# Kernel optimization log

Measured on AMD Instinct MI355X. Metric: run time of the kernel, lower is better.

The kernel has to match this reference:

```python
import jax, jax.numpy as jnp
import numpy as np

T = 5       # fixed temporal factor in the original forward
HEADS = 8
DIM = 512
DIM_HEAD = 64
INNER = HEADS * DIM_HEAD  # 512 (must equal DIM for the masked scatter)


def setup_inputs() -> dict:
    key = jax.random.key(0)
    ks = jax.random.split(key, 8)
    bt, n = 40, 3137  # b=8, t=5; n-1 = 56*56 visual tokens
    x = jax.random.normal(ks[0], (bt, n, DIM), dtype=jnp.float32)
    mask = jax.random.randint(ks[1], (bt, 56, 56), 0, 2).astype(jnp.float32)
    s = 1.0 / np.sqrt(DIM)
    w_vq = jax.random.normal(ks[2], (DIM, INNER), dtype=jnp.float32) * s
    w_vkv = jax.random.normal(ks[3], (DIM, 2 * INNER), dtype=jnp.float32) * s
    w_aqkv = jax.random.normal(ks[4], (DIM, 3 * INNER), dtype=jnp.float32) * s
    w_out = jax.random.normal(ks[5], (INNER, DIM), dtype=jnp.float32) * s
    b_out = jnp.zeros((DIM,), dtype=jnp.float32)
    return {"x": x, "mask": mask, "w_vq": w_vq, "w_vkv": w_vkv,
            "w_aqkv": w_aqkv, "w_out": w_out, "b_out": b_out}


def reference(x, mask, w_vq, w_vkv, w_aqkv, w_out, b_out):
    bt, n, dim = x.shape
    b = bt // T
    nv = n - 1
    dh = DIM_HEAD
    scale = dh ** -0.5

    A = x[:, 0]        # (bt, dim) -- single 'action' token per frame
    V = x[:, 1:]       # (bt, nv, dim)
    m = mask.reshape(bt, nv, 1)

    aq, ak, av = jnp.split(A @ w_aqkv, 3, axis=-1)      # each (bt, INNER)
    vk, vv = jnp.split(V @ w_vkv, 2, axis=-1)           # each (bt, nv, INNER)
    vq = V @ w_vq                                        # (bt, nv, INNER)

    # --- A -> V cross attention: per batch, T A-queries over T*nv V keys ---
    qa = aq.reshape(b, T, HEADS, dh)
    Kv = vk.reshape(b, T * nv, HEADS, dh)
    Vv = vv.reshape(b, T * nv, HEADS, dh)
    av_dots = jnp.einsum('bqhd,bkhd->bhqk', qa, Kv) * scale
    av_attn = jax.nn.softmax(av_dots, axis=-1)
    av_o = jnp.einsum('bhqk,bkhd->bqhd', av_attn, Vv)   # (b, T, H, dh)
    a_out = av_o.reshape(bt, 1, INNER)

    # --- V -> A cross attention with block mask: every V token attends only
    # to its own batch's T A-tokens (the -inf block fill in the original) ---
    Qv = vq.reshape(b, T, nv, HEADS, dh)
    Ka = ak.reshape(b, T, HEADS, dh)
    Va = av.reshape(b, T, HEADS, dh)
    va_dots = jnp.einsum('bfnhd,bkhd->bhfnk', Qv, Ka) * scale
    va_attn = jax.nn.softmax(va_dots, axis=-1)          # softmax over T keys
    va_o = jnp.einsum('bhfnk,bkhd->bfnhd', va_attn, Va)
    v_full = va_o.reshape(bt, nv, INNER)

    # original: scatter attn out into V.clone() then * mask, under no_grad()
    # => masked positions get attention output, others V*0 = 0; detached.
    v_out = jax.lax.stop_gradient(v_full * m)

    out = jnp.concatenate([a_out, v_out], axis=1)       # (bt, n, INNER)
    return out @ w_out + b_out
```

## Files before the change

kernel.cpp:

```cpp
#include <hip/hip_runtime.h>

typedef unsigned short u16;
typedef unsigned int u32;
typedef __attribute__((ext_vector_type(8))) u16 u16x8;
typedef __attribute__((ext_vector_type(8))) __bf16 bf16x8;
typedef __attribute__((ext_vector_type(4))) float f32x4;

__device__ __forceinline__ float b2f(u16 u){ return __uint_as_float(((u32)u)<<16); }
__device__ __forceinline__ u16 f2b(float f){
  u32 b = __float_as_uint(f);
  return (u16)((b + 0x7fffu + ((b>>16)&1u))>>16);
}
__device__ __forceinline__ void gload16(const void* g, void* l){
  __builtin_amdgcn_global_load_lds((__attribute__((address_space(1))) void*)g,
                                   (__attribute__((address_space(3))) void*)l, 16, 0, 0);
}
__device__ __forceinline__ float wred_max(float v){
#pragma unroll
  for (int o=32;o>0;o>>=1) v = fmaxf(v, __shfl_xor(v,o));
  return v;
}
__device__ __forceinline__ float wred_sum(float v){
#pragma unroll
  for (int o=32;o>0;o>>=1) v += __shfl_xor(v,o);
  return v;
}

__global__ void k_cast_x(const float* __restrict__ x, u16* __restrict__ xb, int n8){
  int stride = gridDim.x*blockDim.x;
  for (int i = blockIdx.x*blockDim.x + threadIdx.x; i < n8; i += stride){
    const float4* p = (const float4*)(x + (size_t)i*8);
    float4 a = p[0], b = p[1];
    u16x8 o;
    o[0]=f2b(a.x); o[1]=f2b(a.y); o[2]=f2b(a.z); o[3]=f2b(a.w);
    o[4]=f2b(b.x); o[5]=f2b(b.y); o[6]=f2b(b.z); o[7]=f2b(b.w);
    *(u16x8*)(xb + (size_t)i*8) = o;
  }
}

__global__ void k_prep_w(const float* __restrict__ wvq, const float* __restrict__ wvkv,
                         const float* __restrict__ wout, u16* __restrict__ W1T,
                         u16* __restrict__ WoutT){
  int id = blockIdx.x*blockDim.x + threadIdx.x;
  if (id < 786432){
    int n = id >> 9, k = id & 511;
    float v = (n < 512) ? wvq[k*512 + n] : wvkv[k*1024 + (n-512)];
    W1T[id] = f2b(v);
  } else {
    int j = id - 786432;
    int n = j >> 9, k = j & 511;
    WoutT[j] = f2b(wout[k*512 + n]);
  }
}

__global__ void k_agent_qkv(const float* __restrict__ x, const float* __restrict__ w,
                            float* __restrict__ aqkv){
  int id = blockIdx.x*blockDim.x + threadIdx.x;
  int bt = id / 1536, c = id % 1536;
  const float* xr = x + (size_t)bt*3137*512;
  float s = 0.f;
  for (int k=0;k<512;k++) s += xr[k]*w[k*1536+c];
  aqkv[id] = s;
}

template<int FOUT>
__global__ __launch_bounds__(512, 2) void k_gemm256(
    const u16* __restrict__ A, const u16* __restrict__ BT,
    int M, int N, int K, int NX,
    u16* __restrict__ Cb, float* __restrict__ Cf, const float* __restrict__ bias)
{
  __shared__ __align__(16) char Ls[4][32768];
  const int tid = threadIdx.x;
  const int wid = tid >> 6, lane = tid & 63;
  const int nwg = gridDim.x, orig = blockIdx.x;
  const int q8 = nwg >> 3, r8 = nwg & 7;
  const int xc = orig & 7, sl = orig >> 3;
  const int work = (xc < r8 ? xc*(q8+1) : r8*(q8+1) + (xc-r8)*q8) + sl;
  const int m0 = (work / NX) * 256, n0 = (work % NX) * 256;
  const size_t K2 = (size_t)K * 2;
  const char* Ab = (const char*)A;
  const char* Bb = (const char*)BT;
  size_t asrc[2], bsrc[2];
  const int ad0 = wid*1024, ad1 = 8192 + wid*1024;
#pragma unroll
  for (int i=0;i<2;i++){
    int row = (i*8 + wid)*16 + (lane & 15);
    int koff = (lane >> 4) << 4;
    int ra = m0 + row; if (ra >= M) ra = M - 1;
    asrc[i] = (size_t)ra * K2 + koff;
    bsrc[i] = (size_t)(n0 + row) * K2 + koff;
  }
#define STAGE(s4, ks) { \
    size_t ko = (size_t)(ks) * 64; \
    gload16(Ab + asrc[0] + ko, Ls[s4] + ad0); \
    gload16(Ab + asrc[1] + ko, Ls[s4] + ad1); \
    gload16(Bb + bsrc[0] + ko, Ls[s4] + 16384 + ad0); \
    gload16(Bb + bsrc[1] + ko, Ls[s4] + 16384 + ad1); }

  f32x4 acc[8][4] = {};
  const int awb = (wid >> 2) * 8192;
  const int bwb = 16384 + (wid & 3) * 4096;
  const int NS = K >> 5;
  STAGE(0,0) STAGE(1,1) STAGE(2,2)
  for (int s = 0; s < NS; ++s){
    if (s + 2 < NS)      { asm volatile("s_waitcnt vmcnt(8)" ::: "memory"); }
    else if (s + 1 < NS) { asm volatile("s_waitcnt vmcnt(4)" ::: "memory"); }
    else                 { asm volatile("s_waitcnt vmcnt(0)" ::: "memory"); }
    __builtin_amdgcn_s_barrier();
    __builtin_amdgcn_sched_barrier(0);
    if (s + 3 < NS) STAGE((s+3)&3, s+3)
    const char* base = Ls[s & 3];
    bf16x8 af[8], bfr[4];
#pragma unroll
    for (int i=0;i<4;i++) af[i] = *(const bf16x8*)(base + awb + i*1024 + lane*16);
#pragma unroll
    for (int i=0;i<4;i++) bfr[i] = *(const bf16x8*)(base + bwb + i*1024 + lane*16);
    asm volatile("s_waitcnt lgkmcnt(0)" ::: "memory");
    __builtin_amdgcn_sched_barrier(0);
    __builtin_amdgcn_s_setprio(1);
#pragma unroll
    for (int mr=0;mr<4;mr++)
#pragma unroll
      for (int nc=0;nc<4;nc++)
        acc[mr][nc] = __builtin_amdgcn_mfma_f32_16x16x32_bf16(af[mr], bfr[nc], acc[mr][nc], 0,0,0);
    __builtin_amdgcn_s_setprio(0);
#pragma unroll
    for (int i=4;i<8;i++) af[i] = *(const bf16x8*)(base + awb + i*1024 + lane*16);
    asm volatile("s_waitcnt lgkmcnt(0)" ::: "memory");
    __builtin_amdgcn_sched_barrier(0);
    __builtin_amdgcn_s_setprio(1);
#pragma unroll
    for (int mr=4;mr<8;mr++)
#pragma unroll
      for (int nc=0;nc<4;nc++)
        acc[mr][nc] = __builtin_amdgcn_mfma_f32_16x16x32_bf16(af[mr], bfr[nc], acc[mr][nc], 0,0,0);
    __builtin_amdgcn_s_setprio(0);
  }
#undef STAGE
  const int wm = (wid >> 2) * 128, wn = (wid & 3) * 64;
  if (m0 + 256 <= M){
#pragma unroll
    for (int mr=0;mr<8;mr++){
#pragma unroll
      for (int nc=0;nc<4;nc++){
#pragma unroll
        for (int rg=0;rg<4;rg++){
          int row = m0 + wm + mr*16 + ((lane>>4)<<2) + rg;
          int col = n0 + wn + nc*16 + (lane&15);
          float v = acc[mr][nc][rg];
          if (FOUT) Cf[(size_t)row*N + col] = v + bias[col];
          else      Cb[(size_t)row*N + col] = f2b(v);
        }
      }
    }
  } else {
#pragma unroll
    for (int mr=0;mr<8;mr++){
#pragma unroll
      for (int nc=0;nc<4;nc++){
#pragma unroll
        for (int rg=0;rg<4;rg++){
          int row = m0 + wm + mr*16 + ((lane>>4)<<2) + rg;
          int col = n0 + wn + nc*16 + (lane&15);
          if (row < M){
            float v = acc[mr][nc][rg];
            if (FOUT) Cf[(size_t)row*N + col] = v + bias[col];
            else      Cb[(size_t)row*N + col] = f2b(v);
          }
        }
      }
    }
  }
}

__global__ __launch_bounds__(320) void k_attn_agent(
    const u16* __restrict__ out1, const float* __restrict__ aqkv,
    float* __restrict__ pm, float* __restrict__ pl, float* __restrict__ pacc)
{
  __shared__ __align__(16) char Ksm[16384];
  __shared__ __align__(16) char Vsm[16384];
  const int bid = blockIdx.x;
  const int sp = bid & 15, bh = bid >> 4, b = bh >> 3, h = bh & 7;
  const int tid = threadIdx.x, wid = tid >> 6, lane = tid & 63;
  const int q = wid;
  float qreg[64];
  {
    const float* ap = aqkv + ((size_t)(b*5+q)*1536 + h*64);
#pragma unroll
    for (int d=0; d<64; d++) qreg[d] = ap[d];
  }
  float m = -1e30f, l = 0.f;
  float acc[8] = {0,0,0,0,0,0,0,0};
  const int g0 = sp * 980;
  for (int c = 0; c < 8; c++){
    for (int idx = tid; idx < 2048; idx += 320){
      int arr = idx >> 10, rem = idx & 1023;
      int r = rem >> 3, seg = rem & 7;
      int loc = c*128 + r; if (loc > 979) loc = 979;
      int gk = g0 + loc;
      int tk = gk / 3136, nv = gk - tk*3136;
      size_t grow = (size_t)((b*5+tk)*3137 + 1 + nv)*1536 + (arr ? 1024 : 512) + h*64 + seg*8;
      u16x8 v = *(const u16x8*)(out1 + grow);
      char* dst = arr ? Vsm : Ksm;
      *(u16x8*)(dst + r*128 + ((seg*16) ^ ((r&7)<<4))) = v;
    }
    __syncthreads();
    float s0 = 0.f, s1 = 0.f;
#pragma unroll
    for (int seg=0; seg<8; seg++){
      const int r0 = lane, r1 = 64 + lane;
      u16x8 k0 = *(const u16x8*)(Ksm + r0*128 + ((seg*16) ^ ((r0&7)<<4)));
      u16x8 k1 = *(const u16x8*)(Ksm + r1*128 + ((seg*16) ^ ((r1&7)<<4)));
#pragma unroll
      for (int j=0;j<8;j++){
        s0 += qreg[seg*8+j]*b2f(k0[j]);
        s1 += qreg[seg*8+j]*b2f(k1[j]);
      }
    }
    s0 *= 0.125f; s1 *= 0.125f;
    const int locbase = c*128;
    if (locbase + lane >= 980)      s0 = -1e30f;
    if (locbase + 64 + lane >= 980) s1 = -1e30f;
    float cmax = wred_max(fmaxf(s0, s1));
    float mn = fmaxf(m, cmax);
    float resc = __expf(m - mn);
    float p0 = (s0 > -1e29f) ? __expf(s0 - mn) : 0.f;
    float p1 = (s1 > -1e29f) ? __expf(s1 - mn) : 0.f;
    l = l*resc + wred_sum(p0 + p1);
#pragma unroll
    for (int j=0;j<8;j++) acc[j] *= resc;
    const int g = lane >> 3, cc = lane & 7;
#pragma unroll
    for (int i=0;i<16;i++){
      int k = i*8 + g;
      u16x8 vv = *(const u16x8*)(Vsm + k*128 + ((cc*16) ^ ((k&7)<<4)));
      float p = (i < 8) ? __shfl(p0, k) : __shfl(p1, k-64);
#pragma unroll
      for (int j=0;j<8;j++) acc[j] += p*b2f(vv[j]);
    }
    m = mn;
    __syncthreads();
  }
#pragma unroll
  for (int j=0;j<8;j++){
    float v = acc[j];
    v += __shfl_xor(v, 8); v += __shfl_xor(v, 16); v += __shfl_xor(v, 32);
    acc[j] = v;
  }
  const int base = (bh*16 + sp)*5 + q;
  if (lane == 0){ pm[base] = m; pl[base] = l; }
  if (lane < 8){
    float* pa = pacc + (size_t)base*64 + lane*8;
#pragma unroll
    for (int j=0;j<8;j++) pa[j] = acc[j];
  }
}

__global__ void k_agent_combine(const float* __restrict__ pm, const float* __restrict__ pl,
                                const float* __restrict__ pacc, u16* __restrict__ IN)
{
  const int id = blockIdx.x;
  const int q = id % 5, t2 = id / 5;
  const int h = t2 & 7, b = t2 >> 3;
  const int d = threadIdx.x;
  const int bh = b*8 + h;
  float ms = -1e30f;
#pragma unroll
  for (int s2=0;s2<16;s2++) ms = fmaxf(ms, pm[(bh*16+s2)*5+q]);
  float L = 0.f, o = 0.f;
#pragma unroll
  for (int s2=0;s2<16;s2++){
    int base = (bh*16+s2)*5+q;
    float w = __expf(pm[base]-ms);
    L += w*pl[base];
    o += w*pacc[(size_t)base*64 + d];
  }
  IN[(size_t)(b*5+q)*3137*512 + h*64 + d] = f2b(o / L);
}

__global__ __launch_bounds__(256) void k_attn_frame(
    const u16* __restrict__ out1, const float* __restrict__ aqkv,
    const float* __restrict__ mask, u16* __restrict__ IN)
{
  __shared__ float Ka[5][8][68];
  __shared__ float Va[5][8][68];
  const int b = blockIdx.y;
  const int tid = threadIdx.x;
  for (int i = tid; i < 2560; i += 256){
    int t = i >> 9, rem = i & 511, hh = rem >> 6, d = rem & 63;
    const float* src = aqkv + (size_t)(b*5+t)*1536;
    Ka[t][hh][d] = src[512 + hh*64 + d];
    Va[t][hh][d] = src[1024 + hh*64 + d];
  }
  __syncthreads();
  const int task = blockIdx.x*256 + tid;
  const int h = task & 7, rl = task >> 3;
  const int f = rl / 3136, nv = rl - f*3136;
  const int bt = b*5 + f;
  const size_t r1 = (size_t)bt*3137 + 1 + nv;
  const u16* qp = out1 + r1*1536 + h*64;
  float qf[64];
#pragma unroll
  for (int sg=0; sg<8; sg++){
    u16x8 v = *(const u16x8*)(qp + sg*8);
#pragma unroll
    for (int j=0;j<8;j++) qf[sg*8+j] = b2f(v[j]);
  }
  float sd[5];
#pragma unroll
  for (int t=0;t<5;t++){
    float s = 0.f;
#pragma unroll
    for (int d=0;d<64;d++) s += qf[d]*Ka[t][h][d];
    sd[t] = s*0.125f;
  }
  float mx = sd[0];
#pragma unroll
  for (int t=1;t<5;t++) mx = fmaxf(mx, sd[t]);
  float p[5], ps = 0.f;
#pragma unroll
  for (int t=0;t<5;t++){ p[t] = __expf(sd[t]-mx); ps += p[t]; }
  const float mv = mask[(size_t)bt*3136 + nv] / ps;
  u16* op = IN + r1*512 + h*64;
#pragma unroll
  for (int sg=0; sg<8; sg++){
    u16x8 o;
#pragma unroll
    for (int j=0;j<8;j++){
      const int d = sg*8+j;
      float v = 0.f;
#pragma unroll
      for (int t=0;t<5;t++) v += p[t]*Va[t][h][d];
      o[j] = f2b(v*mv);
    }
    *(u16x8*)(op + sg*8) = o;
  }
}

extern "C" void kernel_launch(void* const* d_in, const int* in_sizes, int n_in,
                              void* d_out, int out_size, void* d_ws, size_t ws_size,
                              hipStream_t stream)
{
  const float* x      = (const float*)d_in[0];
  const float* mask   = (const float*)d_in[1];
  const float* w_vq   = (const float*)d_in[2];
  const float* w_vkv  = (const float*)d_in[3];
  const float* w_aqkv = (const float*)d_in[4];
  const float* w_out  = (const float*)d_in[5];
  const float* b_out  = (const float*)d_in[6];
  float* out = (float*)d_out;
  char* ws = (char*)d_ws;

  constexpr size_t MR = 125480;
  constexpr size_t OFF_XB   = 0;
  constexpr size_t OFF_OUT1 = OFF_XB + MR*512*2;
  constexpr size_t OFF_W1T  = OFF_OUT1 + MR*1536*2;
  constexpr size_t OFF_WOT  = OFF_W1T + 1536*512*2;
  constexpr size_t OFF_AQKV = OFF_WOT + 512*512*2;
  constexpr size_t OFF_PM   = OFF_W1T;
  constexpr size_t OFF_PL   = OFF_PM + 5120*4;
  constexpr size_t OFF_PACC = OFF_PL + 5120*4;

  u16* Xb     = (u16*)(ws + OFF_XB);
  u16* out1   = (u16*)(ws + OFF_OUT1);
  u16* W1T    = (u16*)(ws + OFF_W1T);
  u16* WoutT  = (u16*)(ws + OFF_WOT);
  float* aqkv = (float*)(ws + OFF_AQKV);
  float* pm   = (float*)(ws + OFF_PM);
  float* pl   = (float*)(ws + OFF_PL);
  float* pacc = (float*)(ws + OFF_PACC);

  k_cast_x<<<2048, 256, 0, stream>>>(x, Xb, 8030720);
  k_prep_w<<<4096, 256, 0, stream>>>(w_vq, w_vkv, w_out, W1T, WoutT);
  k_agent_qkv<<<240, 256, 0, stream>>>(x, w_aqkv, aqkv);
  k_gemm256<0><<<2946, 512, 0, stream>>>(Xb, W1T, (int)MR, 1536, 512, 6, out1, nullptr, nullptr);
  k_attn_agent<<<1024, 320, 0, stream>>>(out1, aqkv, pm, pl, pacc);
  k_attn_frame<<<dim3(490,8), 256, 0, stream>>>(out1, aqkv, mask, Xb);
  k_agent_combine<<<320, 64, 0, stream>>>(pm, pl, pacc, Xb);
  k_gemm256<1><<<982, 512, 0, stream>>>(Xb, WoutT, (int)MR, 512, 512, 2, nullptr, out, b_out);
}
```

Before: 811.7 us.

## Software-pipeline LDS fragment loads across K-steps with ping-pong B registers

Restructures the GEMM main loop so the LDS reads for the next K-step (A rows 0-3 and the B fragments) are issued before the second half of the current step's MFMAs. B fragments alternate between two register sets, and the loop is unrolled by two. Partial lgkmcnt waits replace full drains. The aim is to hide LDS read latency behind MFMA work, at the cost of more registers and an assumption that the K-step count is even.

```diff
diff --git a/kernel.cpp b/kernel.cpp
--- a/kernel.cpp
+++ b/kernel.cpp
@@ -101,41 +101,70 @@
   const int awb = (wid >> 2) * 8192;
   const int bwb = 16384 + (wid & 3) * 4096;
   const int NS = K >> 5;
+  bf16x8 af[8], bfE[4], bfO[4];
   STAGE(0,0) STAGE(1,1) STAGE(2,2)
-  for (int s = 0; s < NS; ++s){
-    if (s + 2 < NS)      { asm volatile("s_waitcnt vmcnt(8)" ::: "memory"); }
-    else if (s + 1 < NS) { asm volatile("s_waitcnt vmcnt(4)" ::: "memory"); }
-    else                 { asm volatile("s_waitcnt vmcnt(0)" ::: "memory"); }
-    __builtin_amdgcn_s_barrier();
-    __builtin_amdgcn_sched_barrier(0);
-    if (s + 3 < NS) STAGE((s+3)&3, s+3)
-    const char* base = Ls[s & 3];
-    bf16x8 af[8], bfr[4];
-#pragma unroll
-    for (int i=0;i<4;i++) af[i] = *(const bf16x8*)(base + awb + i*1024 + lane*16);
-#pragma unroll
-    for (int i=0;i<4;i++) bfr[i] = *(const bf16x8*)(base + bwb + i*1024 + lane*16);
-    asm volatile("s_waitcnt lgkmcnt(0)" ::: "memory");
-    __builtin_amdgcn_sched_barrier(0);
-    __builtin_amdgcn_s_setprio(1);
-#pragma unroll
-    for (int mr=0;mr<4;mr++)
-#pragma unroll
-      for (int nc=0;nc<4;nc++)
-        acc[mr][nc] = __builtin_amdgcn_mfma_f32_16x16x32_bf16(af[mr], bfr[nc], acc[mr][nc], 0,0,0);
-    __builtin_amdgcn_s_setprio(0);
-#pragma unroll
-    for (int i=4;i<8;i++) af[i] = *(const bf16x8*)(base + awb + i*1024 + lane*16);
-    asm volatile("s_waitcnt lgkmcnt(0)" ::: "memory");
-    __builtin_amdgcn_sched_barrier(0);
-    __builtin_amdgcn_s_setprio(1);
-#pragma unroll
-    for (int mr=4;mr<8;mr++)
-#pragma unroll
-      for (int nc=0;nc<4;nc++)
-        acc[mr][nc] = __builtin_amdgcn_mfma_f32_16x16x32_bf16(af[mr], bfr[nc], acc[mr][nc], 0,0,0);
-    __builtin_amdgcn_s_setprio(0);
-  }
+  asm volatile("s_waitcnt vmcnt(8)" ::: "memory");
+  __builtin_amdgcn_s_barrier();
+  __builtin_amdgcn_sched_barrier(0);
+  {
+    const char* b0 = Ls[0];
+#pragma unroll
+    for (int i=0;i<4;i++) af[i]  = *(const bf16x8*)(b0 + awb + i*1024 + lane*16);
+#pragma unroll
+    for (int i=0;i<4;i++) bfE[i] = *(const bf16x8*)(b0 + bwb + i*1024 + lane*16);
+  }
+  __builtin_amdgcn_sched_barrier(0);
+
+#define SLOT_BODY(s, CUR, NXT) { \
+    const char* base = Ls[(s) & 3]; \
+    _Pragma("unroll") \
+    for (int i=4;i<8;i++) af[i] = *(const bf16x8*)(base + awb + i*1024 + lane*16); \
+    __builtin_amdgcn_sched_barrier(0); \
+    asm volatile("s_waitcnt lgkmcnt(4)" ::: "memory"); \
+    __builtin_amdgcn_sched_barrier(0); \
+    __builtin_amdgcn_s_setprio(1); \
+    _Pragma("unroll") \
+    for (int mr=0;mr<4;mr++){ \
+      _Pragma("unroll") \
+      for (int nc=0;nc<4;nc++) \
+        acc[mr][nc] = __builtin_amdgcn_mfma_f32_16x16x32_bf16(af[mr], CUR[nc], acc[mr][nc], 0,0,0); \
+    } \
+    __builtin_amdgcn_s_setprio(0); \
+    __builtin_amdgcn_sched_barrier(0); \
+    if ((s) + 1 < NS){ \
+      if ((s) + 2 < NS) { asm volatile("s_waitcnt vmcnt(4)" ::: "memory"); } \
+      else              { asm volatile("s_waitcnt vmcnt(0)" ::: "memory"); } \
+      __builtin_amdgcn_s_barrier(); \
+      __builtin_amdgcn_sched_barrier(0); \
+      if ((s) + 3 < NS) STAGE(((s)+3)&3, (s)+3) \
+      const char* nb = Ls[((s)+1) & 3]; \
+      _Pragma("unroll") \
+      for (int i=0;i<4;i++) af[i]  = *(const bf16x8*)(nb + awb + i*1024 + lane*16); \
+      _Pragma("unroll") \
+      for (int i=0;i<4;i++) NXT[i] = *(const bf16x8*)(nb + bwb + i*1024 + lane*16); \
+      __builtin_amdgcn_sched_barrier(0); \
+      asm volatile("s_waitcnt lgkmcnt(8)" ::: "memory"); \
+      __builtin_amdgcn_sched_barrier(0); \
+    } else { \
+      asm volatile("s_waitcnt lgkmcnt(0)" ::: "memory"); \
+      __builtin_amdgcn_sched_barrier(0); \
+    } \
+    __builtin_amdgcn_s_setprio(1); \
+    _Pragma("unroll") \
+    for (int mr=4;mr<8;mr++){ \
+      _Pragma("unroll") \
+      for (int nc=0;nc<4;nc++) \
+        acc[mr][nc] = __builtin_amdgcn_mfma_f32_16x16x32_bf16(af[mr], CUR[nc], acc[mr][nc], 0,0,0); \
+    } \
+    __builtin_amdgcn_s_setprio(0); \
+    __builtin_amdgcn_sched_barrier(0); \
+  }
+
+  for (int s = 0; s < NS; s += 2){
+    SLOT_BODY(s,   bfE, bfO)
+    SLOT_BODY(s+1, bfO, bfE)
+  }
+#undef SLOT_BODY
 #undef STAGE
   const int wm = (wid >> 2) * 128, wn = (wid & 3) * 64;
   if (m0 + 256 <= M){
```

New measurement: 813.4 us. About the same (+0.2%).

## Split QKV GEMM output into head-major K/V buffers and merge small kernels

Applied to the files above, without the earlier changes.

The first GEMM now writes its output to three buffers: VQ row-major, plus K and V in a per-head layout [h][row][64], so the agent attention reads contiguous 128-byte rows per head instead of strided slices of a 1536-wide row. The cast, weight-prep and agent-QKV kernels are merged into one launch, and the combine step is folded into the frame-attention kernel as extra blocks, which cuts launch count. The cost is a scattered, branchy epilogue in the GEMM with 2-byte stores spread across head planes, which may hurt store coalescing. The partial-result buffers also move to their own workspace region.

```diff
diff --git a/kernel.cpp b/kernel.cpp
--- a/kernel.cpp
+++ b/kernel.cpp
@@ -26,48 +26,51 @@
   return v;
 }
 
-__global__ void k_cast_x(const float* __restrict__ x, u16* __restrict__ xb, int n8){
-  int stride = gridDim.x*blockDim.x;
-  for (int i = blockIdx.x*blockDim.x + threadIdx.x; i < n8; i += stride){
-    const float4* p = (const float4*)(x + (size_t)i*8);
-    float4 a = p[0], b = p[1];
-    u16x8 o;
-    o[0]=f2b(a.x); o[1]=f2b(a.y); o[2]=f2b(a.z); o[3]=f2b(a.w);
-    o[4]=f2b(b.x); o[5]=f2b(b.y); o[6]=f2b(b.z); o[7]=f2b(b.w);
-    *(u16x8*)(xb + (size_t)i*8) = o;
-  }
-}
-
-__global__ void k_prep_w(const float* __restrict__ wvq, const float* __restrict__ wvkv,
-                         const float* __restrict__ wout, u16* __restrict__ W1T,
-                         u16* __restrict__ WoutT){
-  int id = blockIdx.x*blockDim.x + threadIdx.x;
-  if (id < 786432){
-    int n = id >> 9, k = id & 511;
-    float v = (n < 512) ? wvq[k*512 + n] : wvkv[k*1024 + (n-512)];
-    W1T[id] = f2b(v);
+#define MRR 125480
+
+__global__ void k_pre(const float* __restrict__ x, const float* __restrict__ wvq,
+                      const float* __restrict__ wvkv, const float* __restrict__ wout,
+                      const float* __restrict__ waqkv,
+                      u16* __restrict__ xb, u16* __restrict__ W1T,
+                      u16* __restrict__ WoutT, float* __restrict__ aqkv){
+  const int bid = blockIdx.x, tid = threadIdx.x;
+  if (bid < 2048){
+    const int stride = 2048*256;
+    for (int i = bid*256 + tid; i < 8030720; i += stride){
+      const float4* p = (const float4*)(x + (size_t)i*8);
+      float4 a = p[0], b = p[1];
+      u16x8 o;
+      o[0]=f2b(a.x); o[1]=f2b(a.y); o[2]=f2b(a.z); o[3]=f2b(a.w);
+      o[4]=f2b(b.x); o[5]=f2b(b.y); o[6]=f2b(b.z); o[7]=f2b(b.w);
+      *(u16x8*)(xb + (size_t)i*8) = o;
+    }
+  } else if (bid < 6144){
+    int id = (bid-2048)*256 + tid;
+    if (id < 786432){
+      int n = id >> 9, k = id & 511;
+      float v = (n < 512) ? wvq[k*512 + n] : wvkv[k*1024 + (n-512)];
+      W1T[id] = f2b(v);
+    } else {
+      int j = id - 786432;
+      int n = j >> 9, k = j & 511;
+      WoutT[j] = f2b(wout[k*512 + n]);
+    }
   } else {
-    int j = id - 786432;
-    int n = j >> 9, k = j & 511;
-    WoutT[j] = f2b(wout[k*512 + n]);
-  }
-}
-
-__global__ void k_agent_qkv(const float* __restrict__ x, const float* __restrict__ w,
-                            float* __restrict__ aqkv){
-  int id = blockIdx.x*blockDim.x + threadIdx.x;
-  int bt = id / 1536, c = id % 1536;
-  const float* xr = x + (size_t)bt*3137*512;
-  float s = 0.f;
-  for (int k=0;k<512;k++) s += xr[k]*w[k*1536+c];
-  aqkv[id] = s;
+    int id = (bid-6144)*256 + tid;
+    int bt = id / 1536, c = id % 1536;
+    const float* xr = x + (size_t)bt*3137*512;
+    float s = 0.f;
+    for (int k=0;k<512;k++) s += xr[k]*waqkv[k*1536+c];
+    aqkv[id] = s;
+  }
 }
 
 template<int FOUT>
 __global__ __launch_bounds__(512, 2) void k_gemm256(
     const u16* __restrict__ A, const u16* __restrict__ BT,
     int M, int N, int K, int NX,
-    u16* __restrict__ Cb, float* __restrict__ Cf, const float* __restrict__ bias)
+    u16* __restrict__ VQ, u16* __restrict__ KH, u16* __restrict__ VH,
+    float* __restrict__ Cf, const float* __restrict__ bias)
 {
   __shared__ __align__(16) char Ls[4][32768];
   const int tid = threadIdx.x;
@@ -112,7 +115,7 @@
     const char* base = Ls[s & 3];
     bf16x8 af[8], bfr[4];
 #pragma unroll
-    for (int i=0;i<4;i++) af[i] = *(const bf16x8*)(base + awb + i*1024 + lane*16);
+    for (int i=0;i<4;i++) af[i]  = *(const bf16x8*)(base + awb + i*1024 + lane*16);
 #pragma unroll
     for (int i=0;i<4;i++) bfr[i] = *(const bf16x8*)(base + bwb + i*1024 + lane*16);
     asm volatile("s_waitcnt lgkmcnt(0)" ::: "memory");
@@ -138,7 +141,8 @@
   }
 #undef STAGE
   const int wm = (wid >> 2) * 128, wn = (wid & 3) * 64;
-  if (m0 + 256 <= M){
+  if (FOUT == 0){
+    const bool full = (m0 + 256 <= M);
 #pragma unroll
     for (int mr=0;mr<8;mr++){
 #pragma unroll
@@ -147,34 +151,55 @@
         for (int rg=0;rg<4;rg++){
           int row = m0 + wm + mr*16 + ((lane>>4)<<2) + rg;
           int col = n0 + wn + nc*16 + (lane&15);
-          float v = acc[mr][nc][rg];
-          if (FOUT) Cf[(size_t)row*N + col] = v + bias[col];
-          else      Cb[(size_t)row*N + col] = f2b(v);
-        }
-      }
-    }
-  } else {
-#pragma unroll
-    for (int mr=0;mr<8;mr++){
-#pragma unroll
-      for (int nc=0;nc<4;nc++){
-#pragma unroll
-        for (int rg=0;rg<4;rg++){
-          int row = m0 + wm + mr*16 + ((lane>>4)<<2) + rg;
-          int col = n0 + wn + nc*16 + (lane&15);
-          if (row < M){
-            float v = acc[mr][nc][rg];
-            if (FOUT) Cf[(size_t)row*N + col] = v + bias[col];
-            else      Cb[(size_t)row*N + col] = f2b(v);
+          if (full || row < M){
+            u16 ov = f2b(acc[mr][nc][rg]);
+            if (col < 512){
+              VQ[(size_t)row*512 + col] = ov;
+            } else if (col < 1024){
+              int h = (col-512)>>6, d = col&63;
+              KH[((size_t)h*MRR + row)*64 + d] = ov;
+            } else {
+              int h = (col-1024)>>6, d = col&63;
+              VH[((size_t)h*MRR + row)*64 + d] = ov;
+            }
           }
         }
       }
     }
+  } else {
+    if (m0 + 256 <= M){
+#pragma unroll
+      for (int mr=0;mr<8;mr++){
+#pragma unroll
+        for (int nc=0;nc<4;nc++){
+#pragma unroll
+          for (int rg=0;rg<4;rg++){
+            int row = m0 + wm + mr*16 + ((lane>>4)<<2) + rg;
+            int col = n0 + wn + nc*16 + (lane&15);
+            Cf[(size_t)row*N + col] = acc[mr][nc][rg] + bias[col];
+          }
+        }
+      }
+    } else {
+#pragma unroll
+      for (int mr=0;mr<8;mr++){
+#pragma unroll
+        for (int nc=0;nc<4;nc++){
+#pragma unroll
+          for (int rg=0;rg<4;rg++){
+            int row = m0 + wm + mr*16 + ((lane>>4)<<2) + rg;
+            int col = n0 + wn + nc*16 + (lane&15);
+            if (row < M) Cf[(size_t)row*N + col] = acc[mr][nc][rg] + bias[col];
+          }
+        }
+      }
+    }
   }
 }
 
 __global__ __launch_bounds__(320) void k_attn_agent(
-    const u16* __restrict__ out1, const float* __restrict__ aqkv,
+    const u16* __restrict__ KH, const u16* __restrict__ VH,
+    const float* __restrict__ aqkv,
     float* __restrict__ pm, float* __restrict__ pl, float* __restrict__ pacc)
 {
   __shared__ __align__(16) char Ksm[16384];
@@ -192,6 +217,7 @@
   float m = -1e30f, l = 0.f;
   float acc[8] = {0,0,0,0,0,0,0,0};
   const int g0 = sp * 980;
+  const size_t hbase = (size_t)h*MRR;
   for (int c = 0; c < 8; c++){
     for (int idx = tid; idx < 2048; idx += 320){
       int arr = idx >> 10, rem = idx & 1023;
@@ -199,8 +225,9 @@
       int loc = c*128 + r; if (loc > 979) loc = 979;
       int gk = g0 + loc;
       int tk = gk / 3136, nv = gk - tk*3136;
-      size_t grow = (size_t)((b*5+tk)*3137 + 1 + nv)*1536 + (arr ? 1024 : 512) + h*64 + seg*8;
-      u16x8 v = *(const u16x8*)(out1 + grow);
+      size_t row = (size_t)(b*5+tk)*3137 + 1 + nv;
+      const u16* srcp = (arr ? VH : KH) + (hbase + row)*64 + seg*8;
+      u16x8 v = *(const u16x8*)srcp;
       char* dst = arr ? Vsm : Ksm;
       *(u16x8*)(dst + r*128 + ((seg*16) ^ ((r&7)<<4))) = v;
     }
@@ -256,84 +283,84 @@
   }
 }
 
-__global__ void k_agent_combine(const float* __restrict__ pm, const float* __restrict__ pl,
-                                const float* __restrict__ pacc, u16* __restrict__ IN)
+__global__ __launch_bounds__(256) void k_attn_frame(
+    const u16* __restrict__ VQ, const float* __restrict__ aqkv,
+    const float* __restrict__ mask, const float* __restrict__ pm,
+    const float* __restrict__ pl, const float* __restrict__ pacc,
+    u16* __restrict__ IN)
 {
-  const int id = blockIdx.x;
-  const int q = id % 5, t2 = id / 5;
-  const int h = t2 & 7, b = t2 >> 3;
-  const int d = threadIdx.x;
-  const int bh = b*8 + h;
-  float ms = -1e30f;
-#pragma unroll
-  for (int s2=0;s2<16;s2++) ms = fmaxf(ms, pm[(bh*16+s2)*5+q]);
-  float L = 0.f, o = 0.f;
-#pragma unroll
-  for (int s2=0;s2<16;s2++){
-    int base = (bh*16+s2)*5+q;
-    float w = __expf(pm[base]-ms);
-    L += w*pl[base];
-    o += w*pacc[(size_t)base*64 + d];
-  }
-  IN[(size_t)(b*5+q)*3137*512 + h*64 + d] = f2b(o / L);
-}
-
-__global__ __launch_bounds__(256) void k_attn_frame(
-    const u16* __restrict__ out1, const float* __restrict__ aqkv,
-    const float* __restrict__ mask, u16* __restrict__ IN)
-{
-  __shared__ float Ka[5][8][68];
-  __shared__ float Va[5][8][68];
-  const int b = blockIdx.y;
-  const int tid = threadIdx.x;
-  for (int i = tid; i < 2560; i += 256){
-    int t = i >> 9, rem = i & 511, hh = rem >> 6, d = rem & 63;
-    const float* src = aqkv + (size_t)(b*5+t)*1536;
-    Ka[t][hh][d] = src[512 + hh*64 + d];
-    Va[t][hh][d] = src[1024 + hh*64 + d];
-  }
-  __syncthreads();
-  const int task = blockIdx.x*256 + tid;
-  const int h = task & 7, rl = task >> 3;
-  const int f = rl / 3136, nv = rl - f*3136;
-  const int bt = b*5 + f;
-  const size_t r1 = (size_t)bt*3137 + 1 + nv;
-  const u16* qp = out1 + r1*1536 + h*64;
-  float qf[64];
-#pragma unroll
-  for (int sg=0; sg<8; sg++){
-    u16x8 v = *(const u16x8*)(qp + sg*8);
-#pragma unroll
-    for (int j=0;j<8;j++) qf[sg*8+j] = b2f(v[j]);
-  }
-  float sd[5];
-#pragma unroll
-  for (int t=0;t<5;t++){
-    float s = 0.f;
-#pragma unroll
-    for (int d=0;d<64;d++) s += qf[d]*Ka[t][h][d];
-    sd[t] = s*0.125f;
-  }
-  float mx = sd[0];
-#pragma unroll
-  for (int t=1;t<5;t++) mx = fmaxf(mx, sd[t]);
-  float p[5], ps = 0.f;
-#pragma unroll
-  for (int t=0;t<5;t++){ p[t] = __expf(sd[t]-mx); ps += p[t]; }
-  const float mv = mask[(size_t)bt*3136 + nv] / ps;
-  u16* op = IN + r1*512 + h*64;
-#pragma unroll
-  for (int sg=0; sg<8; sg++){
-    u16x8 o;
-#pragma unroll
-    for (int j=0;j<8;j++){
-      const int d = sg*8+j;
-      float v = 0.f;
-#pragma unroll
-      for (int t=0;t<5;t++) v += p[t]*Va[t][h][d];
-      o[j] = f2b(v*mv);
-    }
-    *(u16x8*)(op + sg*8) = o;
+  const int bid = blockIdx.x, tid = threadIdx.x;
+  if (bid < 3920){
+    __shared__ float Ka[5][8][68];
+    __shared__ float Va[5][8][68];
+    const int b = bid / 490, bx = bid % 490;
+    for (int i = tid; i < 2560; i += 256){
+      int t = i >> 9, rem = i & 511, hh = rem >> 6, d = rem & 63;
+      const float* src = aqkv + (size_t)(b*5+t)*1536;
+      Ka[t][hh][d] = src[512 + hh*64 + d];
+      Va[t][hh][d] = src[1024 + hh*64 + d];
+    }
+    __syncthreads();
+    const int task = bx*256 + tid;
+    const int h = task & 7, rl = task >> 3;
+    const int f = rl / 3136, nv = rl - f*3136;
+    const int bt = b*5 + f;
+    const size_t r1 = (size_t)bt*3137 + 1 + nv;
+    const u16* qp = VQ + r1*512 + h*64;
+    float qf[64];
+#pragma unroll
+    for (int sg=0; sg<8; sg++){
+      u16x8 v = *(const u16x8*)(qp + sg*8);
+#pragma unroll
+      for (int j=0;j<8;j++) qf[sg*8+j] = b2f(v[j]);
+    }
+    float sd[5];
+#pragma unroll
+    for (int t=0;t<5;t++){
+      float s = 0.f;
+#pragma unroll
+      for (int d=0;d<64;d++) s += qf[d]*Ka[t][h][d];
+      sd[t] = s*0.125f;
+    }
+    float mx = sd[0];
+#pragma unroll
+    for (int t=1;t<5;t++) mx = fmaxf(mx, sd[t]);
+    float p[5], ps = 0.f;
+#pragma unroll
+    for (int t=0;t<5;t++){ p[t] = __expf(sd[t]-mx); ps += p[t]; }
+    const float mv = mask[(size_t)bt*3136 + nv] / ps;
+    u16* op = IN + r1*512 + h*64;
+#pragma unroll
+    for (int sg=0; sg<8; sg++){
+      u16x8 o;
+#pragma unroll
+      for (int j=0;j<8;j++){
+        const int d = sg*8+j;
+        float v = 0.f;
+#pragma unroll
+        for (int t=0;t<5;t++) v += p[t]*Va[t][h][d];
+        o[j] = f2b(v*mv);
+      }
+      *(u16x8*)(op + sg*8) = o;
+    }
+  } else {
+    const int id = (bid - 3920)*4 + (tid >> 6);
+    const int d = tid & 63;
+    const int q = id % 5, t2 = id / 5;
+    const int h = t2 & 7, b = t2 >> 3;
+    const int bh = b*8 + h;
+    float ms = -1e30f;
+#pragma unroll
+    for (int s2=0;s2<16;s2++) ms = fmaxf(ms, pm[(bh*16+s2)*5+q]);
+    float L = 0.f, o = 0.f;
+#pragma unroll
+    for (int s2=0;s2<16;s2++){
+      int base = (bh*16+s2)*5+q;
+      float w = __expf(pm[base]-ms);
+      L += w*pl[base];
+      o += w*pacc[(size_t)base*64 + d];
+    }
+    IN[(size_t)(b*5+q)*3137*512 + h*64 + d] = f2b(o / L);
   }
 }
 
@@ -353,16 +380,20 @@
 
   constexpr size_t MR = 125480;
   constexpr size_t OFF_XB   = 0;
-  constexpr size_t OFF_OUT1 = OFF_XB + MR*512*2;
-  constexpr size_t OFF_W1T  = OFF_OUT1 + MR*1536*2;
+  constexpr size_t OFF_VQ   = OFF_XB + MR*512*2;
+  constexpr size_t OFF_KH   = OFF_VQ + MR*512*2;
+  constexpr size_t OFF_VH   = OFF_KH + MR*512*2;
+  constexpr size_t OFF_W1T  = OFF_VH + MR*512*2;
   constexpr size_t OFF_WOT  = OFF_W1T + 1536*512*2;
   constexpr size_t OFF_AQKV = OFF_WOT + 512*512*2;
-  constexpr size_t OFF_PM   = OFF_W1T;
+  constexpr size_t OFF_PM   = OFF_AQKV + 40*1536*4;
   constexpr size_t OFF_PL   = OFF_PM + 5120*4;
   constexpr size_t OFF_PACC = OFF_PL + 5120*4;
 
   u16* Xb     = (u16*)(ws + OFF_XB);
-  u16* out1   = (u16*)(ws + OFF_OUT1);
+  u16* VQ     = (u16*)(ws + OFF_VQ);
+  u16* KH     = (u16*)(ws + OFF_KH);
+  u16* VH     = (u16*)(ws + OFF_VH);
   u16* W1T    = (u16*)(ws + OFF_W1T);
   u16* WoutT  = (u16*)(ws + OFF_WOT);
   float* aqkv = (float*)(ws + OFF_AQKV);
@@ -370,12 +401,11 @@
   float* pl   = (float*)(ws + OFF_PL);
   float* pacc = (float*)(ws + OFF_PACC);
 
-  k_cast_x<<<2048, 256, 0, stream>>>(x, Xb, 8030720);
-  k_prep_w<<<4096, 256, 0, stream>>>(w_vq, w_vkv, w_out, W1T, WoutT);
-  k_agent_qkv<<<240, 256, 0, stream>>>(x, w_aqkv, aqkv);
-  k_gemm256<0><<<2946, 512, 0, stream>>>(Xb, W1T, (int)MR, 1536, 512, 6, out1, nullptr, nullptr);
-  k_attn_agent<<<1024, 320, 0, stream>>>(out1, aqkv, pm, pl, pacc);
-  k_attn_frame<<<dim3(490,8), 256, 0, stream>>>(out1, aqkv, mask, Xb);
-  k_agent_combine<<<320, 64, 0, stream>>>(pm, pl, pacc, Xb);
-  k_gemm256<1><<<982, 512, 0, stream>>>(Xb, WoutT, (int)MR, 512, 512, 2, nullptr, out, b_out);
-}
+  k_pre<<<6384, 256, 0, stream>>>(x, w_vq, w_vkv, w_out, w_aqkv, Xb, W1T, WoutT, aqkv);
+  k_gemm256<0><<<2946, 512, 0, stream>>>(Xb, W1T, (int)MR, 1536, 512, 6,
+                                         VQ, KH, VH, nullptr, nullptr);
+  k_attn_agent<<<1024, 320, 0, stream>>>(KH, VH, aqkv, pm, pl, pacc);
+  k_attn_frame<<<4000, 256, 0, stream>>>(VQ, aqkv, mask, pm, pl, pacc, Xb);
+  k_gemm256<1><<<982, 512, 0, stream>>>(Xb, WoutT, (int)MR, 512, 512, 2,
+                                        nullptr, nullptr, nullptr, out, b_out);
+}
```

New measurement: 859.9 us. +5.9%, slower.

## Merge prep kernels, fold agent combine into frame kernel, interleave K/V columns

Applied to the files above, without the earlier changes.

Merges the x cast, weight transpose and agent QKV projection into one launch, and folds the agent-combine step into the frame-attention kernel as extra blocks. This cuts the number of kernel launches and the gaps between them. The K/V weight columns are reordered so that each head's K and V sit next to each other (128 contiguous columns), which lets the agent attention load both in one contiguous read per row. The partial-softmax buffers get their own workspace region instead of aliasing W1T, because W1T is now written in the same phase.

```diff
diff --git a/kernel.cpp b/kernel.cpp
--- a/kernel.cpp
+++ b/kernel.cpp
@@ -26,41 +26,49 @@
   return v;
 }
 
-__global__ void k_cast_x(const float* __restrict__ x, u16* __restrict__ xb, int n8){
-  int stride = gridDim.x*blockDim.x;
-  for (int i = blockIdx.x*blockDim.x + threadIdx.x; i < n8; i += stride){
-    const float4* p = (const float4*)(x + (size_t)i*8);
-    float4 a = p[0], b = p[1];
-    u16x8 o;
-    o[0]=f2b(a.x); o[1]=f2b(a.y); o[2]=f2b(a.z); o[3]=f2b(a.w);
-    o[4]=f2b(b.x); o[5]=f2b(b.y); o[6]=f2b(b.z); o[7]=f2b(b.w);
-    *(u16x8*)(xb + (size_t)i*8) = o;
-  }
-}
-
-__global__ void k_prep_w(const float* __restrict__ wvq, const float* __restrict__ wvkv,
-                         const float* __restrict__ wout, u16* __restrict__ W1T,
-                         u16* __restrict__ WoutT){
-  int id = blockIdx.x*blockDim.x + threadIdx.x;
-  if (id < 786432){
-    int n = id >> 9, k = id & 511;
-    float v = (n < 512) ? wvq[k*512 + n] : wvkv[k*1024 + (n-512)];
-    W1T[id] = f2b(v);
+
+__global__ void k_pre(const float* __restrict__ x, const float* __restrict__ wvq,
+                      const float* __restrict__ wvkv, const float* __restrict__ wout,
+                      const float* __restrict__ waqkv,
+                      u16* __restrict__ xb, u16* __restrict__ W1T,
+                      u16* __restrict__ WoutT, float* __restrict__ aqkv){
+  const int bid = blockIdx.x, tid = threadIdx.x;
+  if (bid < 2048){
+    const int stride = 2048*256;
+    for (int i = bid*256 + tid; i < 8030720; i += stride){
+      const float4* p = (const float4*)(x + (size_t)i*8);
+      float4 a = p[0], b = p[1];
+      u16x8 o;
+      o[0]=f2b(a.x); o[1]=f2b(a.y); o[2]=f2b(a.z); o[3]=f2b(a.w);
+      o[4]=f2b(b.x); o[5]=f2b(b.y); o[6]=f2b(b.z); o[7]=f2b(b.w);
+      *(u16x8*)(xb + (size_t)i*8) = o;
+    }
+  } else if (bid < 6144){
+    int id = (bid-2048)*256 + tid;
+    if (id < 786432){
+      int n = id >> 9, k = id & 511;
+      float v;
+      if (n < 512){
+        v = wvq[k*512 + n];
+      } else {
+        int j = n - 512, h = j >> 7, r = j & 127;
+        int c2 = (r < 64) ? (h*64 + r) : (512 + h*64 + (r - 64));
+        v = wvkv[k*1024 + c2];
+      }
+      W1T[id] = f2b(v);
+    } else {
+      int j = id - 786432;
+      int n = j >> 9, k = j & 511;
+      WoutT[j] = f2b(wout[k*512 + n]);
+    }
   } else {
-    int j = id - 786432;
-    int n = j >> 9, k = j & 511;
-    WoutT[j] = f2b(wout[k*512 + n]);
-  }
-}
-
-__global__ void k_agent_qkv(const float* __restrict__ x, const float* __restrict__ w,
-                            float* __restrict__ aqkv){
-  int id = blockIdx.x*blockDim.x + threadIdx.x;
-  int bt = id / 1536, c = id % 1536;
-  const float* xr = x + (size_t)bt*3137*512;
-  float s = 0.f;
-  for (int k=0;k<512;k++) s += xr[k]*w[k*1536+c];
-  aqkv[id] = s;
+    int id = (bid-6144)*256 + tid;
+    int bt = id / 1536, c = id % 1536;
+    const float* xr = x + (size_t)bt*3137*512;
+    float s = 0.f;
+    for (int k=0;k<512;k++) s += xr[k]*waqkv[k*1536+c];
+    aqkv[id] = s;
+  }
 }
 
 template<int FOUT>
@@ -112,7 +120,7 @@
     const char* base = Ls[s & 3];
     bf16x8 af[8], bfr[4];
 #pragma unroll
-    for (int i=0;i<4;i++) af[i] = *(const bf16x8*)(base + awb + i*1024 + lane*16);
+    for (int i=0;i<4;i++) af[i]  = *(const bf16x8*)(base + awb + i*1024 + lane*16);
 #pragma unroll
     for (int i=0;i<4;i++) bfr[i] = *(const bf16x8*)(base + bwb + i*1024 + lane*16);
     asm volatile("s_waitcnt lgkmcnt(0)" ::: "memory");
@@ -194,14 +202,14 @@
   const int g0 = sp * 980;
   for (int c = 0; c < 8; c++){
     for (int idx = tid; idx < 2048; idx += 320){
-      int arr = idx >> 10, rem = idx & 1023;
-      int r = rem >> 3, seg = rem & 7;
+      int r = idx >> 4, g = idx & 15;
       int loc = c*128 + r; if (loc > 979) loc = 979;
       int gk = g0 + loc;
       int tk = gk / 3136, nv = gk - tk*3136;
-      size_t grow = (size_t)((b*5+tk)*3137 + 1 + nv)*1536 + (arr ? 1024 : 512) + h*64 + seg*8;
+      size_t grow = (size_t)((b*5+tk)*3137 + 1 + nv)*1536 + 512 + h*128 + g*8;
       u16x8 v = *(const u16x8*)(out1 + grow);
-      char* dst = arr ? Vsm : Ksm;
+      char* dst = (g < 8) ? Ksm : Vsm;
+      int seg = g & 7;
       *(u16x8*)(dst + r*128 + ((seg*16) ^ ((r&7)<<4))) = v;
     }
     __syncthreads();
@@ -256,84 +264,84 @@
   }
 }
 
-__global__ void k_agent_combine(const float* __restrict__ pm, const float* __restrict__ pl,
-                                const float* __restrict__ pacc, u16* __restrict__ IN)
-{
-  const int id = blockIdx.x;
-  const int q = id % 5, t2 = id / 5;
-  const int h = t2 & 7, b = t2 >> 3;
-  const int d = threadIdx.x;
-  const int bh = b*8 + h;
-  float ms = -1e30f;
-#pragma unroll
-  for (int s2=0;s2<16;s2++) ms = fmaxf(ms, pm[(bh*16+s2)*5+q]);
-  float L = 0.f, o = 0.f;
-#pragma unroll
-  for (int s2=0;s2<16;s2++){
-    int base = (bh*16+s2)*5+q;
-    float w = __expf(pm[base]-ms);
-    L += w*pl[base];
-    o += w*pacc[(size_t)base*64 + d];
-  }
-  IN[(size_t)(b*5+q)*3137*512 + h*64 + d] = f2b(o / L);
-}
-
 __global__ __launch_bounds__(256) void k_attn_frame(
     const u16* __restrict__ out1, const float* __restrict__ aqkv,
-    const float* __restrict__ mask, u16* __restrict__ IN)
+    const float* __restrict__ mask, const float* __restrict__ pm,
+    const float* __restrict__ pl, const float* __restrict__ pacc,
+    u16* __restrict__ IN)
 {
-  __shared__ float Ka[5][8][68];
-  __shared__ float Va[5][8][68];
-  const int b = blockIdx.y;
-  const int tid = threadIdx.x;
-  for (int i = tid; i < 2560; i += 256){
-    int t = i >> 9, rem = i & 511, hh = rem >> 6, d = rem & 63;
-    const float* src = aqkv + (size_t)(b*5+t)*1536;
-    Ka[t][hh][d] = src[512 + hh*64 + d];
-    Va[t][hh][d] = src[1024 + hh*64 + d];
-  }
-  __syncthreads();
-  const int task = blockIdx.x*256 + tid;
-  const int h = task & 7, rl = task >> 3;
-  const int f = rl / 3136, nv = rl - f*3136;
-  const int bt = b*5 + f;
-  const size_t r1 = (size_t)bt*3137 + 1 + nv;
-  const u16* qp = out1 + r1*1536 + h*64;
-  float qf[64];
-#pragma unroll
-  for (int sg=0; sg<8; sg++){
-    u16x8 v = *(const u16x8*)(qp + sg*8);
-#pragma unroll
-    for (int j=0;j<8;j++) qf[sg*8+j] = b2f(v[j]);
-  }
-  float sd[5];
-#pragma unroll
-  for (int t=0;t<5;t++){
-    float s = 0.f;
-#pragma unroll
-    for (int d=0;d<64;d++) s += qf[d]*Ka[t][h][d];
-    sd[t] = s*0.125f;
-  }
-  float mx = sd[0];
-#pragma unroll
-  for (int t=1;t<5;t++) mx = fmaxf(mx, sd[t]);
-  float p[5], ps = 0.f;
-#pragma unroll
-  for (int t=0;t<5;t++){ p[t] = __expf(sd[t]-mx); ps += p[t]; }
-  const float mv = mask[(size_t)bt*3136 + nv] / ps;
-  u16* op = IN + r1*512 + h*64;
-#pragma unroll
-  for (int sg=0; sg<8; sg++){
-    u16x8 o;
-#pragma unroll
-    for (int j=0;j<8;j++){
-      const int d = sg*8+j;
-      float v = 0.f;
-#pragma unroll
-      for (int t=0;t<5;t++) v += p[t]*Va[t][h][d];
-      o[j] = f2b(v*mv);
-    }
-    *(u16x8*)(op + sg*8) = o;
+  const int bid = blockIdx.x, tid = threadIdx.x;
+  if (bid < 3920){
+    __shared__ float Ka[5][8][68];
+    __shared__ float Va[5][8][68];
+    const int b = bid / 490, bx = bid % 490;
+    for (int i = tid; i < 2560; i += 256){
+      int t = i >> 9, rem = i & 511, hh = rem >> 6, d = rem & 63;
+      const float* src = aqkv + (size_t)(b*5+t)*1536;
+      Ka[t][hh][d] = src[512 + hh*64 + d];
+      Va[t][hh][d] = src[1024 + hh*64 + d];
+    }
+    __syncthreads();
+    const int task = bx*256 + tid;
+    const int h = task & 7, rl = task >> 3;
+    const int f = rl / 3136, nv = rl - f*3136;
+    const int bt = b*5 + f;
+    const size_t r1 = (size_t)bt*3137 + 1 + nv;
+    const u16* qp = out1 + r1*1536 + h*64;
+    float qf[64];
+#pragma unroll
+    for (int sg=0; sg<8; sg++){
+      u16x8 v = *(const u16x8*)(qp + sg*8);
+#pragma unroll
+      for (int j=0;j<8;j++) qf[sg*8+j] = b2f(v[j]);
+    }
+    float sd[5];
+#pragma unroll
+    for (int t=0;t<5;t++){
+      float s = 0.f;
+#pragma unroll
+      for (int d=0;d<64;d++) s += qf[d]*Ka[t][h][d];
+      sd[t] = s*0.125f;
+    }
+    float mx = sd[0];
+#pragma unroll
+    for (int t=1;t<5;t++) mx = fmaxf(mx, sd[t]);
+    float p[5], ps = 0.f;
+#pragma unroll
+    for (int t=0;t<5;t++){ p[t] = __expf(sd[t]-mx); ps += p[t]; }
+    const float mv = mask[(size_t)bt*3136 + nv] / ps;
+    u16* op = IN + r1*512 + h*64;
+#pragma unroll
+    for (int sg=0; sg<8; sg++){
+      u16x8 o;
+#pragma unroll
+      for (int j=0;j<8;j++){
+        const int d = sg*8+j;
+        float v = 0.f;
+#pragma unroll
+        for (int t=0;t<5;t++) v += p[t]*Va[t][h][d];
+        o[j] = f2b(v*mv);
+      }
+      *(u16x8*)(op + sg*8) = o;
+    }
+  } else {
+    const int id = (bid - 3920)*4 + (tid >> 6);
+    const int d = tid & 63;
+    const int q = id % 5, t2 = id / 5;
+    const int h = t2 & 7, b = t2 >> 3;
+    const int bh = b*8 + h;
+    float ms = -1e30f;
+#pragma unroll
+    for (int s2=0;s2<16;s2++) ms = fmaxf(ms, pm[(bh*16+s2)*5+q]);
+    float L = 0.f, o = 0.f;
+#pragma unroll
+    for (int s2=0;s2<16;s2++){
+      int base = (bh*16+s2)*5+q;
+      float w = __expf(pm[base]-ms);
+      L += w*pl[base];
+      o += w*pacc[(size_t)base*64 + d];
+    }
+    IN[(size_t)(b*5+q)*3137*512 + h*64 + d] = f2b(o / L);
   }
 }
 
@@ -357,7 +365,7 @@
   constexpr size_t OFF_W1T  = OFF_OUT1 + MR*1536*2;
   constexpr size_t OFF_WOT  = OFF_W1T + 1536*512*2;
   constexpr size_t OFF_AQKV = OFF_WOT + 512*512*2;
-  constexpr size_t OFF_PM   = OFF_W1T;
+  constexpr size_t OFF_PM   = OFF_AQKV + 40*1536*4;
   constexpr size_t OFF_PL   = OFF_PM + 5120*4;
   constexpr size_t OFF_PACC = OFF_PL + 5120*4;
 
@@ -370,12 +378,11 @@
   float* pl   = (float*)(ws + OFF_PL);
   float* pacc = (float*)(ws + OFF_PACC);
 
-  k_cast_x<<<2048, 256, 0, stream>>>(x, Xb, 8030720);
-  k_prep_w<<<4096, 256, 0, stream>>>(w_vq, w_vkv, w_out, W1T, WoutT);
-  k_agent_qkv<<<240, 256, 0, stream>>>(x, w_aqkv, aqkv);
-  k_gemm256<0><<<2946, 512, 0, stream>>>(Xb, W1T, (int)MR, 1536, 512, 6, out1, nullptr, nullptr);
+  k_pre<<<6384, 256, 0, stream>>>(x, w_vq, w_vkv, w_out, w_aqkv, Xb, W1T, WoutT, aqkv);
+  k_gemm256<0><<<2946, 512, 0, stream>>>(Xb, W1T, (int)MR, 1536, 512, 6,
+                                         out1, nullptr, nullptr);
   k_attn_agent<<<1024, 320, 0, stream>>>(out1, aqkv, pm, pl, pacc);
-  k_attn_frame<<<dim3(490,8), 256, 0, stream>>>(out1, aqkv, mask, Xb);
-  k_agent_combine<<<320, 64, 0, stream>>>(pm, pl, pacc, Xb);
-  k_gemm256<1><<<982, 512, 0, stream>>>(Xb, WoutT, (int)MR, 512, 512, 2, nullptr, out, b_out);
-}
+  k_attn_frame<<<4000, 256, 0, stream>>>(out1, aqkv, mask, pm, pl, pacc, Xb);
+  k_gemm256<1><<<982, 512, 0, stream>>>(Xb, WoutT, (int)MR, 512, 512, 2,
+                                        nullptr, out, b_out);
+}
```

After: 784.3 us. -3.4%, faster.
